# Optimization experiments

Measured on AMD Instinct MI355X. Metric: run time of the kernel, lower is better.

Reference implementation:

```python
import jax, jax.numpy as jnp
import numpy as np
import math

NLAT, NLON, LMAX, MMAX = 128, 256, 50, 50
K = 3  # three_nn

# ---- precompute: Clenshaw-Curtis quadrature (torch_harmonics 'equiangular') ----
def _cc_nodes_weights(n):
    Nn = n - 1
    theta = np.pi * np.arange(n) / Nn
    v = np.zeros(n)
    for k in range(1, Nn // 2 + 1):
        b = 1.0 if 2 * k == Nn else 2.0
        v += b * np.cos(2 * k * theta) / (4 * k * k - 1)
    w = (2.0 / Nn) * (1.0 - v)
    w[0] *= 0.5
    w[-1] *= 0.5
    return np.cos(theta), w

# ---- precompute: orthonormal associated Legendre P_l^m(cos theta), csphase ----
def _legpoly(lmax, mmax, cost):
    sint = np.sqrt(np.clip(1.0 - cost ** 2, 0.0, None))
    p = np.zeros((mmax, lmax, cost.shape[0]))
    pmm = np.full(cost.shape[0], np.sqrt(1.0 / (4.0 * np.pi)))
    for m in range(mmax):
        if m > 0:
            pmm = -pmm * np.sqrt((2.0 * m + 1.0) / (2.0 * m)) * sint
        p[m, m] = pmm
        if m + 1 < lmax:
            p[m, m + 1] = np.sqrt(2.0 * m + 3.0) * cost * pmm
        for l in range(m + 2, lmax):
            a = np.sqrt((4.0 * l * l - 1.0) / (l * l - m * m))
            b = np.sqrt(((2.0 * l + 1.0) * (l - 1 + m) * (l - 1 - m)) / ((2.0 * l - 3.0) * (l * l - m * m)))
            p[m, l] = a * cost * p[m, l - 1] - b * p[m, l - 2]
    return p

_cost, _w = _cc_nodes_weights(NLAT)
_PCTW = jnp.asarray((_legpoly(LMAX, MMAX, _cost) * _w[None, None, :]).astype(np.float32))  # (mmax,lmax,nlat)

_gx, _gy = np.meshgrid(np.arange(NLAT), np.arange(-NLAT, NLAT), indexing='ij')
_GRID = jnp.asarray((np.stack([_gx.ravel(), _gy.ravel()], -1) / NLAT * np.pi).astype(np.float32))  # (M,2)

_RECTW = jnp.asarray(np.exp(-(LMAX - np.arange(1, LMAX + 1)) ** 2 / (2.0 * LMAX ** 2)).astype(np.float32))  # (lmax,)


def to_spherical(coords):
    # coords: (B,N,3) -> r:(B,N), sph:(B,N,2) = [arccos(x/r), azimuth in [0,2pi)]
    sq = coords ** 2
    pn = jnp.sqrt(jnp.flip(jnp.cumsum(jnp.flip(sq, -1), -1), -1))  # pn[...,i] = ||coords[...,i:]||
    r = pn[..., 0]
    phi = jnp.arccos(coords[..., :-2] / pn[..., :-2])
    a = jnp.arccos(coords[..., -2] / pn[..., -2])
    phi_final = a + (2.0 * math.pi - 2.0 * a) * (coords[..., -1] < 0)
    return r, jnp.concatenate([phi, phi_final[..., None]], axis=-1)


def interp_to_grid(coords):
    # spherical transform + 3-NN (squared dists) + distance-weighted interpolation onto the lat/lon grid
    r, sph = to_spherical(coords)
    sph = sph.at[..., 1].add(-math.pi)
    # brute-force pairwise squared distances grid(M,2) vs sph(B,N,2): (B,M,N)
    d2 = (jnp.sum(_GRID ** 2, -1)[None, :, None] + jnp.sum(sph ** 2, -1)[:, None, :]
          - 2.0 * jnp.einsum('md,bnd->bmn', _GRID, sph))
    _, idx = jax.lax.top_k(-jax.lax.stop_gradient(d2), K)  # (B,M,K), ascending distance
    sel = jax.vmap(lambda s, i: s[i])(sph, idx)            # (B,M,K,2)
    fsel = jax.vmap(lambda f, i: f[i])(r, idx)             # (B,M,K)
    dk = jnp.sum((_GRID[None, :, None, :] - sel) ** 2, -1)  # recompute selected sq-dists (differentiable)
    w = dk / jnp.sum(dk, -1, keepdims=True)                # weights = dist / sum(dist), as in source
    return jnp.sum(fsel * w, -1).reshape(-1, NLAT, NLON)


def sht_real(x):
    # RealSHT (equiangular, ortho): rfft(norm='forward')*2pi, then Legendre*quadrature einsum; real part only
    xf = jnp.fft.rfft(x, axis=-1)[..., :MMAX] * (2.0 * math.pi / NLON)
    return jnp.einsum('bkm,mlk->blm', jnp.real(xf).astype(jnp.float32), _PCTW)  # (B,lmax,mmax)


def setup_inputs() -> dict:
    key = jax.random.key(0)
    k1, k2 = jax.random.split(key)
    pred = jax.random.normal(k1, (2, 2048, 3), dtype=jnp.float32)
    target = jax.random.normal(k2, (2, 2048, 3), dtype=jnp.float32)
    return {"pred": pred, "target": target}


def reference(pred, target):
    pc = sht_real(interp_to_grid(pred))
    tc = sht_real(interp_to_grid(target))
    return jnp.mean(jnp.sum((pc - tc) ** 2 * _RECTW[None, :, None], axis=(1, 2)))
```

## Files before the change

kernel.cpp:

```cpp
#include <hip/hip_runtime.h>
#include <math.h>

#define PI_D 3.14159265358979323846
#define PIF  3.14159265358979323846f
#define NLAT 128
#define NLON 256
#define LMAX 50
#define MMAX 50
#define NPTS 2048
#define NBT 16
#define NBA 32
#define NBIN (NBT * NBA)
#define WBIN 0.19634954084936207f
#define INVW 5.092958178940651f
#define BIG 1e30f
#define KMASK 0xFFFFF800u

__device__ __forceinline__ void insert3(float kf, float& k0, float& k1, float& k2) {
    float n1 = __builtin_amdgcn_fmed3f(kf, k0, k1);
    float n2 = __builtin_amdgcn_fmed3f(kf, k1, k2);
    k0 = fminf(kf, k0);
    k1 = n1;
    k2 = n2;
}

__device__ __forceinline__ float mkkey(float gt, float gl, float2 tl, int idx) {
    float dt = gt - tl.x, dl = gl - tl.y;
    float d = fmaf(dt, dt, dl * dl);
    return __uint_as_float((__float_as_uint(d) & KMASK) | (unsigned)idx);
}

__global__ __launch_bounds__(256) void fused_main(
    const float* __restrict__ pred, const float* __restrict__ tgt,
    float* __restrict__ pctwT, float* __restrict__ fre, float* __restrict__ out) {

    __shared__ float2 s_btl[NPTS];
    __shared__ float  s_br[NPTS];
    __shared__ int    s_cnt[NBIN];
    __shared__ int    s_off[NBIN + 1];
    __shared__ float  ctab[NLON];
    __shared__ float  row[NLON];
    __shared__ float  part[200];

    int bid = blockIdx.x;
    int t = threadIdx.x;

    if (bid >= 512) {
        int k = bid - 512;
        if (k == 0 && t == 0) out[0] = 0.0f;
        if (t < MMAX) {
            int m = t;
            double theta = PI_D * (double)k / 127.0;
            double cost = cos(theta);
            double sint = sqrt(fmax(1.0 - cost * cost, 0.0));
            double c2 = cos(2.0 * theta);
            double two_c2 = 2.0 * c2;
            double cp = 1.0, cc = c2, v = 0.0;
            for (int tt = 1; tt <= 63; ++tt) {
                v += 2.0 * cc / (double)(4 * tt * tt - 1);
                double cn = two_c2 * cc - cp;
                cp = cc;
                cc = cn;
            }
            double w = (2.0 / 127.0) * (1.0 - v);
            if (k == 0 || k == 127) w *= 0.5;

            double pmm = sqrt(1.0 / (4.0 * PI_D));
            for (int i = 1; i <= m; ++i)
                pmm = -pmm * sqrt((2.0 * (double)i + 1.0) / (2.0 * (double)i)) * sint;

            float* o = pctwT + (size_t)k * MMAX + m;
            for (int l = 0; l < m; ++l) o[(size_t)l * NLAT * MMAX] = 0.0f;
            o[(size_t)m * NLAT * MMAX] = (float)(pmm * w);
            double plm2 = pmm, plm1 = 0.0;
            if (m + 1 < LMAX) {
                plm1 = sqrt(2.0 * (double)m + 3.0) * cost * pmm;
                o[(size_t)(m + 1) * NLAT * MMAX] = (float)(plm1 * w);
            }
            for (int l = m + 2; l < LMAX; ++l) {
                double ll = (double)l;
                double denom = ll * ll - (double)(m * m);
                double a = sqrt((4.0 * ll * ll - 1.0) / denom);
                double b = sqrt(((2.0 * ll + 1.0) * (double)(l - 1 + m) * (double)(l - 1 - m)) /
                                ((2.0 * ll - 3.0) * denom));
                double p = a * cost * plm1 - b * plm2;
                o[(size_t)l * NLAT * MMAX] = (float)(p * w);
                plm2 = plm1;
                plm1 = p;
            }
        }
        return;
    }

    int f = bid >> 7;
    int lat = bid & 127;
    const float* src = ((f < 2) ? pred : tgt) + (size_t)(f & 1) * NPTS * 3;

    s_cnt[t] = 0;
    s_cnt[t + 256] = 0;
    ctab[t] = (float)cos(2.0 * PI_D * (double)t / (double)NLON);
    __syncthreads();

    float pth[8], paz[8], pr[8];
    int pbin[8];
#pragma unroll
    for (int i = 0; i < 8; ++i) {
        int n = t + 256 * i;
        float x = src[3 * n], y = src[3 * n + 1], z = src[3 * n + 2];
        float s1 = z * z;
        float s2 = s1 + y * y;
        float s3 = s2 + x * x;
        float r = sqrtf(s3);
        float rho = sqrtf(s2);
        float th = acosf(x / r);
        float a = acosf(y / rho);
        float az = (z < 0.0f) ? (a + (2.0f * PIF - 2.0f * a)) : a;
        az -= PIF;
        int bt = min(max((int)(th * INVW), 0), NBT - 1);
        int ba = min(max((int)((az + PIF) * INVW), 0), NBA - 1);
        int b = bt * NBA + ba;
        pth[i] = th; paz[i] = az; pr[i] = r; pbin[i] = b;
        atomicAdd(&s_cnt[b], 1);
    }
    __syncthreads();

    if (t == 0) s_off[NBIN] = NPTS;
    if (t < 64) {
        int base = t * 8;
        int loc[8];
        int run = 0;
#pragma unroll
        for (int i = 0; i < 8; ++i) { loc[i] = run; run += s_cnt[base + i]; }
        int x = run;
#pragma unroll
        for (int d = 1; d < 64; d <<= 1) {
            int y = __shfl_up(x, d);
            if (t >= d) x += y;
        }
        int ex = x - run;
#pragma unroll
        for (int i = 0; i < 8; ++i) s_off[base + i] = ex + loc[i];
    }
    __syncthreads();
    s_cnt[t] = s_off[t];
    s_cnt[t + 256] = s_off[t + 256];
    __syncthreads();
#pragma unroll
    for (int i = 0; i < 8; ++i) {
        int pos = atomicAdd(&s_cnt[pbin[i]], 1);
        s_btl[pos] = make_float2(pth[i], paz[i]);
        s_br[pos] = pr[i];
    }
    __syncthreads();

    int j = t;
    float gt = (float)((double)lat * PI_D / 128.0);
    float gl = (float)(((double)j - 128.0) * PI_D / 128.0);
    float glp = gl + PIF;
    int bt0 = lat >> 3;
    int ba0 = j >> 3;

    auto scan_seg = [&](int i, int i1, float& q0, float& q1, float& q2) {
        for (; i + 4 <= i1; i += 4) {
            float2 a0 = s_btl[i];
            float2 a1 = s_btl[i + 1];
            float2 a2 = s_btl[i + 2];
            float2 a3 = s_btl[i + 3];
            insert3(mkkey(gt, gl, a0, i), q0, q1, q2);
            insert3(mkkey(gt, gl, a1, i + 1), q0, q1, q2);
            insert3(mkkey(gt, gl, a2, i + 2), q0, q1, q2);
            insert3(mkkey(gt, gl, a3, i + 3), q0, q1, q2);
        }
        for (; i < i1; ++i)
            insert3(mkkey(gt, gl, s_btl[i], i), q0, q1, q2);
    };

    float k0 = BIG, k1 = BIG, k2 = BIG;

    {
        int rtl = max(bt0 - 1, 0), rth = min(bt0 + 1, NBT - 1);
        int bal = max(ba0 - 1, 0), bah = min(ba0 + 1, NBA - 1);
        for (int bt = rtl; bt <= rth; ++bt)
            scan_seg(s_off[bt * NBA + bal], s_off[bt * NBA + bah + 1], k0, k1, k2);
    }

    bool done;
    {
        float safe = BIG;
        if (bt0 - 1 > 0)       safe = fminf(safe, gt - (float)(bt0 - 1) * WBIN);
        if (bt0 + 1 < NBT - 1) safe = fminf(safe, (float)(bt0 + 2) * WBIN - gt);
        if (ba0 - 1 > 0)       safe = fminf(safe, glp - (float)(ba0 - 1) * WBIN);
        if (ba0 + 1 < NBA - 1) safe = fminf(safe, (float)(ba0 + 2) * WBIN - glp);
        done = (k2 <= safe * safe);
    }

    if (__any(!done)) {
        float q0 = BIG, q1 = BIG, q2 = BIG;
        int lo = bt0, hi = bt0;
        scan_seg(s_off[bt0 * NBA], s_off[(bt0 + 1) * NBA], q0, q1, q2);
        while (true) {
            float safe = BIG;
            if (lo > 0)       safe = fminf(safe, gt - (float)lo * WBIN);
            if (hi < NBT - 1) safe = fminf(safe, (float)(hi + 1) * WBIN - gt);
            if (__all(q2 <= safe * safe)) break;
            if (lo == 0 && hi == NBT - 1) break;
            if (lo > 0) {
                --lo;
                scan_seg(s_off[lo * NBA], s_off[(lo + 1) * NBA], q0, q1, q2);
            }
            if (hi < NBT - 1) {
                ++hi;
                scan_seg(s_off[hi * NBA], s_off[(hi + 1) * NBA], q0, q1, q2);
            }
        }
        if (!done) { k0 = q0; k1 = q1; k2 = q2; }
    }

    {
        int i0 = __float_as_uint(k0) & 0x7FF;
        int i1 = __float_as_uint(k1) & 0x7FF;
        int i2 = __float_as_uint(k2) & 0x7FF;
        float2 p0 = s_btl[i0];
        float2 p1 = s_btl[i1];
        float2 p2 = s_btl[i2];
        float dt0 = gt - p0.x, dl0 = gl - p0.y;
        float dt1 = gt - p1.x, dl1 = gl - p1.y;
        float dt2 = gt - p2.x, dl2 = gl - p2.y;
        float d0 = fmaf(dt0, dt0, dl0 * dl0);
        float d1 = fmaf(dt1, dt1, dl1 * dl1);
        float d2 = fmaf(dt2, dt2, dl2 * dl2);
        float s = d0 + d1 + d2;
        row[j] = (d0 * s_br[i0] + d1 * s_br[i1] + d2 * s_br[i2]) / s;
    }
    __syncthreads();

    if (t < 200) {
        int mm = t >> 2, q = t & 3;
        int bs = q * 64;
        float acc = 0.0f;
        int p = (bs * mm) & (NLON - 1);
        for (int i = 0; i < 64; ++i) {
            acc += row[bs + i] * ctab[p];
            p = (p + mm) & (NLON - 1);
        }
        part[t] = acc;
    }
    __syncthreads();
    if (t < MMAX) {
        const float* pp = part + t * 4;
        fre[(f * NLAT + lat) * MMAX + t] =
            ((pp[0] + pp[1]) + (pp[2] + pp[3])) * (float)(2.0 * PI_D / (double)NLON);
    }
}

__global__ __launch_bounds__(256) void contract_loss(const float* __restrict__ fre,
                                                     const float* __restrict__ pctwT,
                                                     float* __restrict__ out) {
    int b = blockIdx.x / LMAX;
    int l = blockIdx.x % LMAX;
    int mm = threadIdx.x & 63;
    int kq = threadIdx.x >> 6;
    __shared__ float sp[4][64], st_[4][64];
    float pc = 0.0f, tc = 0.0f;
    if (mm < MMAX) {
        const float* pw = pctwT + ((size_t)l * NLAT + kq * 32) * MMAX + mm;
        const float* fp = fre + ((size_t)b * NLAT + kq * 32) * MMAX + mm;
        const float* ft = fre + ((size_t)(2 + b) * NLAT + kq * 32) * MMAX + mm;
#pragma unroll 8
        for (int k = 0; k < 32; ++k) {
            float w = pw[k * MMAX];
            pc += fp[k * MMAX] * w;
            tc += ft[k * MMAX] * w;
        }
    }
    sp[kq][mm] = pc;
    st_[kq][mm] = tc;
    __syncthreads();
    if (threadIdx.x < 64) {
        int m2 = threadIdx.x;
        float pcs = (sp[0][m2] + sp[1][m2]) + (sp[2][m2] + sp[3][m2]);
        float tcs = (st_[0][m2] + st_[1][m2]) + (st_[2][m2] + st_[3][m2]);
        float diff = pcs - tcs;
        double dl_ = (double)(49 - l);
        float rw = (float)exp(-(dl_ * dl_) / 5000.0);
        float contrib = (m2 < MMAX) ? diff * diff * rw * 0.5f : 0.0f;
        for (int off = 32; off > 0; off >>= 1) contrib += __shfl_down(contrib, off);
        if (m2 == 0) atomicAdd(out, contrib);
    }
}

extern "C" void kernel_launch(void* const* d_in, const int* in_sizes, int n_in,
                              void* d_out, int out_size, void* d_ws, size_t ws_size,
                              hipStream_t stream) {
    const float* pred = (const float*)d_in[0];
    const float* tgt = (const float*)d_in[1];
    float* ws = (float*)d_ws;

    float* pctwT = ws;
    float* fre   = ws + 320000;
    float* out = (float*)d_out;

    fused_main<<<640, 256, 0, stream>>>(pred, tgt, pctwT, fre, out);
    contract_loss<<<2 * LMAX, 256, 0, stream>>>(fre, pctwT, out);
}
```

Baseline: 90.64 us.

## Split Legendre table into float kernel and use wave-uniform kNN bin windows

Moves the Legendre/quadrature table computation out of the fused kNN kernel into a separate 64-thread kernel and switches it from double to float math. In the kNN search, each 64-lane wave now scans one shared azimuth bin window instead of a per-thread 3x3 window, which removes divergence but makes each thread scan more points. The fallback search also starts from the three latitude rows rather than one. The float table may lose accuracy at high degree, and adding a third launch adds launch overhead.

```diff
diff --git a/kernel.cpp b/kernel.cpp
--- a/kernel.cpp
+++ b/kernel.cpp
@@ -30,10 +30,57 @@
     return __uint_as_float((__float_as_uint(d) & KMASK) | (unsigned)idx);
 }
 
-__global__ __launch_bounds__(256) void fused_main(
-    const float* __restrict__ pred, const float* __restrict__ tgt,
-    float* __restrict__ pctwT, float* __restrict__ fre, float* __restrict__ out) {
-
+__global__ __launch_bounds__(64) void pctw_kernel(float* __restrict__ pctwT,
+                                                  float* __restrict__ out) {
+    int k = blockIdx.x;
+    int m = threadIdx.x;
+    if (k == 0 && m == 0) out[0] = 0.0f;
+    if (m >= MMAX) return;
+
+    double thd = PI_D * (double)k / 127.0;
+    float cost = (float)cos(thd);
+    float sint = (float)sin(thd);
+
+    float c2 = (float)cos(2.0 * thd);
+    float two_c2 = 2.0f * c2;
+    float cp = 1.0f, cc = c2, v = 0.0f;
+    for (int tt = 1; tt <= 63; ++tt) {
+        v += 2.0f * cc / (float)(4 * tt * tt - 1);
+        float cn = two_c2 * cc - cp;
+        cp = cc;
+        cc = cn;
+    }
+    float w = (2.0f / 127.0f) * (1.0f - v);
+    if (k == 0 || k == 127) w *= 0.5f;
+
+    float pmm = sqrtf(1.0f / (4.0f * PIF));
+    for (int i = 1; i <= m; ++i)
+        pmm = -pmm * sqrtf((2.0f * (float)i + 1.0f) / (2.0f * (float)i)) * sint;
+
+    float* o = pctwT + (size_t)k * MMAX + m;
+    for (int l = 0; l < m; ++l) o[(size_t)l * NLAT * MMAX] = 0.0f;
+    o[(size_t)m * NLAT * MMAX] = pmm * w;
+    float plm2 = pmm, plm1 = 0.0f;
+    if (m + 1 < LMAX) {
+        plm1 = sqrtf(2.0f * (float)m + 3.0f) * cost * pmm;
+        o[(size_t)(m + 1) * NLAT * MMAX] = plm1 * w;
+    }
+    for (int l = m + 2; l < LMAX; ++l) {
+        float fl = (float)l;
+        float denom = fl * fl - (float)(m * m);
+        float a = sqrtf((4.0f * fl * fl - 1.0f) / denom);
+        float b = sqrtf(((2.0f * fl + 1.0f) * (float)(l - 1 + m) * (float)(l - 1 - m)) /
+                        ((2.0f * fl - 3.0f) * denom));
+        float p = a * cost * plm1 - b * plm2;
+        o[(size_t)l * NLAT * MMAX] = p * w;
+        plm2 = plm1;
+        plm1 = p;
+    }
+}
+
+__global__ __launch_bounds__(256) void knn_kernel(const float* __restrict__ pred,
+                                                  const float* __restrict__ tgt,
+                                                  float* __restrict__ fre) {
     __shared__ float2 s_btl[NPTS];
     __shared__ float  s_br[NPTS];
     __shared__ int    s_cnt[NBIN];
@@ -44,54 +91,6 @@
 
     int bid = blockIdx.x;
     int t = threadIdx.x;
-
-    if (bid >= 512) {
-        int k = bid - 512;
-        if (k == 0 && t == 0) out[0] = 0.0f;
-        if (t < MMAX) {
-            int m = t;
-            double theta = PI_D * (double)k / 127.0;
-            double cost = cos(theta);
-            double sint = sqrt(fmax(1.0 - cost * cost, 0.0));
-            double c2 = cos(2.0 * theta);
-            double two_c2 = 2.0 * c2;
-            double cp = 1.0, cc = c2, v = 0.0;
-            for (int tt = 1; tt <= 63; ++tt) {
-                v += 2.0 * cc / (double)(4 * tt * tt - 1);
-                double cn = two_c2 * cc - cp;
-                cp = cc;
-                cc = cn;
-            }
-            double w = (2.0 / 127.0) * (1.0 - v);
-            if (k == 0 || k == 127) w *= 0.5;
-
-            double pmm = sqrt(1.0 / (4.0 * PI_D));
-            for (int i = 1; i <= m; ++i)
-                pmm = -pmm * sqrt((2.0 * (double)i + 1.0) / (2.0 * (double)i)) * sint;
-
-            float* o = pctwT + (size_t)k * MMAX + m;
-            for (int l = 0; l < m; ++l) o[(size_t)l * NLAT * MMAX] = 0.0f;
-            o[(size_t)m * NLAT * MMAX] = (float)(pmm * w);
-            double plm2 = pmm, plm1 = 0.0;
-            if (m + 1 < LMAX) {
-                plm1 = sqrt(2.0 * (double)m + 3.0) * cost * pmm;
-                o[(size_t)(m + 1) * NLAT * MMAX] = (float)(plm1 * w);
-            }
-            for (int l = m + 2; l < LMAX; ++l) {
-                double ll = (double)l;
-                double denom = ll * ll - (double)(m * m);
-                double a = sqrt((4.0 * ll * ll - 1.0) / denom);
-                double b = sqrt(((2.0 * ll + 1.0) * (double)(l - 1 + m) * (double)(l - 1 - m)) /
-                                ((2.0 * ll - 3.0) * denom));
-                double p = a * cost * plm1 - b * plm2;
-                o[(size_t)l * NLAT * MMAX] = (float)(p * w);
-                plm2 = plm1;
-                plm1 = p;
-            }
-        }
-        return;
-    }
-
     int f = bid >> 7;
     int lat = bid & 127;
     const float* src = ((f < 2) ? pred : tgt) + (size_t)(f & 1) * NPTS * 3;
@@ -154,34 +153,22 @@
     __syncthreads();
 
     int j = t;
+    int wv = t >> 6;
     float gt = (float)((double)lat * PI_D / 128.0);
     float gl = (float)(((double)j - 128.0) * PI_D / 128.0);
     float glp = gl + PIF;
     int bt0 = lat >> 3;
-    int ba0 = j >> 3;
-
-    auto scan_seg = [&](int i, int i1, float& q0, float& q1, float& q2) {
-        for (; i + 4 <= i1; i += 4) {
-            float2 a0 = s_btl[i];
-            float2 a1 = s_btl[i + 1];
-            float2 a2 = s_btl[i + 2];
-            float2 a3 = s_btl[i + 3];
-            insert3(mkkey(gt, gl, a0, i), q0, q1, q2);
-            insert3(mkkey(gt, gl, a1, i + 1), q0, q1, q2);
-            insert3(mkkey(gt, gl, a2, i + 2), q0, q1, q2);
-            insert3(mkkey(gt, gl, a3, i + 3), q0, q1, q2);
-        }
+    int lo_a = max(wv * 8 - 1, 0);
+    int hi_a = min(wv * 8 + 8, NBA - 1);
+    int rlo = max(bt0 - 1, 0), rhi = min(bt0 + 1, NBT - 1);
+
+    float k0 = BIG, k1 = BIG, k2 = BIG;
+    for (int bt = rlo; bt <= rhi; ++bt) {
+        int i = s_off[bt * NBA + lo_a];
+        int i1 = s_off[bt * NBA + hi_a + 1];
+#pragma unroll 4
         for (; i < i1; ++i)
-            insert3(mkkey(gt, gl, s_btl[i], i), q0, q1, q2);
-    };
-
-    float k0 = BIG, k1 = BIG, k2 = BIG;
-
-    {
-        int rtl = max(bt0 - 1, 0), rth = min(bt0 + 1, NBT - 1);
-        int bal = max(ba0 - 1, 0), bah = min(ba0 + 1, NBA - 1);
-        for (int bt = rtl; bt <= rth; ++bt)
-            scan_seg(s_off[bt * NBA + bal], s_off[bt * NBA + bah + 1], k0, k1, k2);
+            insert3(mkkey(gt, gl, s_btl[i], i), k0, k1, k2);
     }
 
     bool done;
@@ -189,28 +176,38 @@
         float safe = BIG;
         if (bt0 - 1 > 0)       safe = fminf(safe, gt - (float)(bt0 - 1) * WBIN);
         if (bt0 + 1 < NBT - 1) safe = fminf(safe, (float)(bt0 + 2) * WBIN - gt);
-        if (ba0 - 1 > 0)       safe = fminf(safe, glp - (float)(ba0 - 1) * WBIN);
-        if (ba0 + 1 < NBA - 1) safe = fminf(safe, (float)(ba0 + 2) * WBIN - glp);
+        if (lo_a > 0)          safe = fminf(safe, glp - (float)lo_a * WBIN);
+        if (hi_a < NBA - 1)    safe = fminf(safe, (float)(hi_a + 1) * WBIN - glp);
         done = (k2 <= safe * safe);
     }
 
     if (__any(!done)) {
         float q0 = BIG, q1 = BIG, q2 = BIG;
-        int lo = bt0, hi = bt0;
-        scan_seg(s_off[bt0 * NBA], s_off[(bt0 + 1) * NBA], q0, q1, q2);
+        int lo = rlo, hi = rhi;
+        for (int bt = rlo; bt <= rhi; ++bt) {
+            int i = s_off[bt * NBA], i1 = s_off[(bt + 1) * NBA];
+#pragma unroll 4
+            for (; i < i1; ++i)
+                insert3(mkkey(gt, gl, s_btl[i], i), q0, q1, q2);
+        }
         while (true) {
-            float safe = BIG;
-            if (lo > 0)       safe = fminf(safe, gt - (float)lo * WBIN);
-            if (hi < NBT - 1) safe = fminf(safe, (float)(hi + 1) * WBIN - gt);
-            if (__all(q2 <= safe * safe)) break;
-            if (lo == 0 && hi == NBT - 1) break;
+            float sf = BIG;
+            if (lo > 0)       sf = fminf(sf, gt - (float)lo * WBIN);
+            if (hi < NBT - 1) sf = fminf(sf, (float)(hi + 1) * WBIN - gt);
+            if (__all(q2 <= sf * sf) || (lo == 0 && hi == NBT - 1)) break;
             if (lo > 0) {
                 --lo;
-                scan_seg(s_off[lo * NBA], s_off[(lo + 1) * NBA], q0, q1, q2);
+                int i = s_off[lo * NBA], i1 = s_off[(lo + 1) * NBA];
+#pragma unroll 4
+                for (; i < i1; ++i)
+                    insert3(mkkey(gt, gl, s_btl[i], i), q0, q1, q2);
             }
             if (hi < NBT - 1) {
                 ++hi;
-                scan_seg(s_off[hi * NBA], s_off[(hi + 1) * NBA], q0, q1, q2);
+                int i = s_off[hi * NBA], i1 = s_off[(hi + 1) * NBA];
+#pragma unroll 4
+                for (; i < i1; ++i)
+                    insert3(mkkey(gt, gl, s_btl[i], i), q0, q1, q2);
             }
         }
         if (!done) { k0 = q0; k1 = q1; k2 = q2; }
@@ -300,6 +297,7 @@
     float* fre   = ws + 320000;
     float* out = (float*)d_out;
 
-    fused_main<<<640, 256, 0, stream>>>(pred, tgt, pctwT, fre, out);
+    knn_kernel<<<512, 256, 0, stream>>>(pred, tgt, fre);
+    pctw_kernel<<<NLAT, 64, 0, stream>>>(pctwT, out);
     contract_loss<<<2 * LMAX, 256, 0, stream>>>(fre, pctwT, out);
 }
```

Result: slower. 107.8 us (+18.9%).
